# Kernel optimization log

Measured on AMD Instinct MI355X. Metric: run time of the kernel, lower is better.

Reference implementation:

```python
import jax, jax.numpy as jnp
from jax import lax
import numpy as np

L, B, N, D = 3, 64, 64, 64
E = 2 * D + 1  # per-edge feature dim: [state_i, state_j, w_ij]


def _build_edge_weights(n):
    # ring lattice (k=6) + distance-decaying random long-range links, symmetrized
    k = min(6, n // 4)
    ew = np.zeros((n, n), dtype=np.float32)
    for i in range(n):
        for j in range(1, k // 2 + 1):
            ew[i, (i + j) % n] = 1.0
            ew[i, (i - j) % n] = 1.0
    rng = np.random.default_rng(42)
    r = rng.random((n, n))
    for i in range(n):
        for j in range(n):
            if i != j and ew[i, j] == 0.0:
                dist = min(abs(i - j), n - abs(i - j))
                if r[i, j] < 0.1 / (dist + 1):
                    ew[i, j] = 0.5
    ew = (ew + ew.T) / 2.0
    return jnp.asarray(ew)


def setup_inputs() -> dict:
    key = jax.random.key(0)
    k1, k2, k3, k4 = jax.random.split(key, 4)
    x = jax.random.normal(k1, (B, N, D), dtype=jnp.float32)
    edge_weights = _build_edge_weights(N)
    W_msg = jax.random.normal(k2, (L, N, N, E, D), dtype=jnp.float32) * 0.05
    b_msg = jnp.zeros((L, N, N, D), dtype=jnp.float32)
    W_upd = jax.random.normal(k3, (L, 2 * D, D), dtype=jnp.float32) * 0.05
    b_upd = jnp.zeros((L, D), dtype=jnp.float32)
    W_out = jax.random.normal(k4, (D, D), dtype=jnp.float32) * 0.05
    b_out = jnp.zeros((D,), dtype=jnp.float32)
    return {"x": x, "edge_weights": edge_weights, "W_msg": W_msg, "b_msg": b_msg,
            "W_upd": W_upd, "b_upd": b_upd, "W_out": W_out, "b_out": b_out}


def reference(x, edge_weights, W_msg, b_msg, W_upd, b_upd, W_out, b_out):
    Bn, Nn, Dn = x.shape
    adj = (edge_weights > 0).astype(x.dtype)          # (N, N)
    deg = adj.sum(axis=1)                              # (N,)
    mask = adj[None, :, :, None]                       # (1, N, N, 1)
    s = x
    for l in range(W_msg.shape[0]):
        # per-edge features [state_i, state_j, w_ij] -> (B, N, N, 2D+1)
        feat_i = jnp.broadcast_to(s[:, :, None, :], (Bn, Nn, Nn, Dn))
        feat_j = jnp.broadcast_to(s[:, None, :, :], (Bn, Nn, Nn, Dn))
        w = jnp.broadcast_to(edge_weights[None, :, :, None], (Bn, Nn, Nn, 1))
        feat = jnp.concatenate([feat_i, feat_j, w], axis=-1)
        # distinct Dense per edge: grouped GEMM over the (i, j) edge grid
        msg = jnp.einsum('bije,ijed->bijd', feat, W_msg[l]) + b_msg[l]
        msg = msg * mask                               # only existing edges message
        agg = msg.sum(axis=2)                          # (B, N, D) sum over senders j
        upd = jnp.concatenate([s, agg], axis=-1) @ W_upd[l] + b_upd[l]
        s = 0.9 * upd + 0.1 * s                        # constraint_factor = 0.1
        # sequential topological constraint: blend each node toward current
        # neighbor average (node i sees already-updated nodes < i)
        def step(state, i):
            nbr_sum = jnp.einsum('j,bjd->bd', adj[i], state)
            avg = nbr_sum / jnp.maximum(deg[i], 1.0)
            new_i = jnp.where(deg[i] > 0, 0.95 * state[:, i] + 0.05 * avg, state[:, i])
            return state.at[:, i].set(new_i), None
        s, _ = lax.scan(step, s, jnp.arange(Nn))
    # degree-centrality weighted readout
    c = edge_weights.sum(axis=1)
    c = c / (c.sum() + 1e-8)
    g = (s * c[None, :, None]).sum(axis=1)             # (B, D)
    return g @ W_out + b_out
```

## Files before the change

### kernel.cpp

```cpp
#include <hip/hip_runtime.h>

namespace {

constexpr int B = 64, N = 64, D = 64, E = 2 * D + 1;
constexpr int NBLK = 256;
constexpr int NTH  = 512;
constexpr int LMAX = 3;
constexpr size_t MAXSLOT = 1024;

__device__ __forceinline__ float4 f4ld(const float* p) { return *(const float4*)p; }
__device__ __forceinline__ void f4acc(float4& a, const float4 b) {
  a.x += b.x; a.y += b.y; a.z += b.z; a.w += b.w;
}

__device__ __forceinline__ void gridbar(unsigned* set, unsigned* nxcd, int lead) {
  asm volatile("s_waitcnt vmcnt(0)" ::: "memory");
  __syncthreads();
  if (threadIdx.x == 0) {
    const int g = blockIdx.x;
    unsigned* leaf  = set + (size_t)(g & 7) * 16;
    unsigned* root  = set + 8 * 16;
    unsigned* root2 = set + 9 * 16;
    __hip_atomic_fetch_add(leaf, 1u, __ATOMIC_RELAXED, __HIP_MEMORY_SCOPE_AGENT);
    if (g < 8) {
      while (__hip_atomic_load(leaf, __ATOMIC_RELAXED, __HIP_MEMORY_SCOPE_AGENT)
             < (unsigned)(NBLK / 8))
        __builtin_amdgcn_s_sleep(2);
      __hip_atomic_fetch_add(root, 1u, __ATOMIC_RELAXED, __HIP_MEMORY_SCOPE_AGENT);
    }
    while (__hip_atomic_load(root, __ATOMIC_RELAXED, __HIP_MEMORY_SCOPE_AGENT) < 8u)
      __builtin_amdgcn_s_sleep(2);
    if (lead) {
      __threadfence();
      __hip_atomic_fetch_add(root2, 1u, __ATOMIC_RELAXED, __HIP_MEMORY_SCOPE_AGENT);
    }
    const unsigned K =
        __hip_atomic_load(nxcd, __ATOMIC_RELAXED, __HIP_MEMORY_SCOPE_AGENT);
    while (__hip_atomic_load(root2, __ATOMIC_RELAXED, __HIP_MEMORY_SCOPE_AGENT) < K)
      __builtin_amdgcn_s_sleep(2);
  }
  __syncthreads();
}

constexpr int OF_WU    = 32768;
constexpr int OF_TB    = 49152;
constexpr int OF_NBR4  = OF_TB;
constexpr int OF_DEG   = OF_TB + 1024;
constexpr int OF_CW    = OF_TB + 1280;
constexpr int OF_CNT   = OF_TB + 1536;
constexpr int OF_RB    = OF_TB + 1792;
constexpr int OF_BTMP  = OF_TB + 2048;
constexpr int OF_NE    = OF_TB + 2304;
constexpr int OF_EI    = OF_TB + 2320;
constexpr int OF_NFULL = OF_TB + 4368;
constexpr int POOLSZ   = 57856;

__global__ __launch_bounds__(NTH) void k_fused(
    const float* __restrict__ x,
    const float* __restrict__ ew,
    const float* __restrict__ Wm,
    const float* __restrict__ bm,
    const float* __restrict__ Wu,
    const float* __restrict__ bu,
    const float* __restrict__ Wo,
    const float* __restrict__ bo,
    float* __restrict__ out,
    char* __restrict__ ws, int L)
{
  unsigned* bar  = (unsigned*)ws;
  unsigned* nxcd = bar + 960;
  char* p = ws + 4096;
  float* sbuf0   = (float*)p; p += (size_t)B * N * D * 4;
  float* sbuf1   = (float*)p; p += (size_t)B * N * D * 4;
  float* selfm   = (float*)p; p += (size_t)LMAX * N * B * D * 4;
  float* msgBuf  = (float*)p; p += (size_t)LMAX * MAXSLOT * B * D * 4;
  float* sw1     = (float*)p; p += (size_t)(LMAX - 1) * N * D * D * 4;
  float* baseB   = (float*)p;

  __shared__ __align__(16) char pool[POOLSZ];
  float (*aT)[64] = (float(*)[64])pool;
  float* wLds  = (float*)(pool + 16384);
  uint4* nbr4L = (uint4*)(pool + OF_NBR4);
  float* degL  = (float*)(pool + OF_DEG);
  float* cwL   = (float*)(pool + OF_CW);
  int*   cntL  = (int*)(pool + OF_CNT);
  int*   rbL   = (int*)(pool + OF_RB);
  float* baseTmp = (float*)(pool + OF_BTMP);
  int*   neL   = (int*)(pool + OF_NE);
  unsigned short* eiL = (unsigned short*)(pool + OF_EI);
  unsigned char* nfullL = (unsigned char*)(pool + OF_NFULL);

  const int g = blockIdx.x, t = threadIdx.x;

  int lead = 0;
  if (t == 0) {
    unsigned xcd = 0;
    asm volatile("s_getreg_b32 %0, hwreg(HW_REG_XCC_ID)" : "=s"(xcd));
    unsigned* elect = bar + 832 + (size_t)(xcd & 7) * 16;
    if (__hip_atomic_fetch_add(elect, 1u, __ATOMIC_RELAXED,
                               __HIP_MEMORY_SCOPE_AGENT) == 0u) {
      lead = 1;
      __hip_atomic_fetch_add(nxcd, 1u, __ATOMIC_RELAXED,
                             __HIP_MEMORY_SCOPE_AGENT);
    }
  }

  {
    float* ewL = (float*)pool;
#pragma unroll
    for (int r = 0; r < 2; ++r)
      ((float4*)ewL)[r * NTH + t] = ((const float4*)ew)[r * NTH + t];
    __syncthreads();
    if (t < 64) {
      float rowsum = 0.f; int rc = 0;
      for (int j = 0; j < N; ++j) {
        const float v = ewL[t * N + j];
        rowsum += v; rc += (v > 0.f) ? 1 : 0;
      }
      int pre = rc;
#pragma unroll
      for (int off = 1; off < 64; off <<= 1) {
        int v = __shfl_up(pre, off, 64);
        if (t >= off) pre += v;
      }
      const int base = pre - rc;
      rbL[t] = base;
      unsigned long long lo = 0ull, hi = 0ull; int c = 0;
      for (int j = 0; j < N; ++j) {
        const float v = ewL[t * N + j];
        if (v > 0.f) {
          eiL[base + c] = (unsigned short)((t << 6) | j);
          if (c < 8)       lo |= (unsigned long long)j << (c * 8);
          else if (c < 16) hi |= (unsigned long long)j << ((c - 8) * 8);
          nfullL[t * 64 + c] = (unsigned char)j;
          ++c;
        }
      }
      uint4 w4;
      w4.x = (unsigned)lo; w4.y = (unsigned)(lo >> 32);
      w4.z = (unsigned)hi; w4.w = (unsigned)(hi >> 32);
      nbr4L[t] = w4; cntL[t] = c; degL[t] = (float)c;
      float tot = rowsum;
#pragma unroll
      for (int off = 32; off >= 1; off >>= 1) tot += __shfl_xor(tot, off, 64);
      cwL[t] = rowsum / (tot + 1e-8f);
      if (t == 63) *neL = base + rc;
    }
    __syncthreads();
  }
  const int ne = *neL;

  for (int l = 0; l < L; ++l) {
    const float* scur = (l == 0) ? x : ((l & 1) ? sbuf1 : sbuf0);
    float* sout = (l & 1) ? sbuf0 : sbuf1;
    float* msgl  = msgBuf + (size_t)l * MAXSLOT * B * D;
    float* selfl = selfm + (size_t)l * N * B * D;
    const bool LAST = (l == L - 1);

    {
      const int U = ne + N;
      for (int u = g; u < U; u += NBLK) {
        const bool self = (u >= ne);
        int i, jj; float* dst;
        if (self) { i = u - ne; jj = i; dst = selfl + (size_t)i * B * D; }
        else {
          const int e = eiL[u]; i = e >> 6; jj = e & 63;
          dst = msgl + (size_t)u * B * D;
        }
        {
          const int bb = t >> 3, q = t & 7;
          const float* ps = scur + ((size_t)(bb * N + jj)) * D + q * 8;
          const float4 v0 = f4ld(ps), v1 = f4ld(ps + 4);
          const int k0 = q * 8;
          aT[k0 + 0][bb] = v0.x; aT[k0 + 1][bb] = v0.y;
          aT[k0 + 2][bb] = v0.z; aT[k0 + 3][bb] = v0.w;
          aT[k0 + 4][bb] = v1.x; aT[k0 + 5][bb] = v1.y;
          aT[k0 + 6][bb] = v1.z; aT[k0 + 7][bb] = v1.w;
        }
        if (!self) {
          const int e = eiL[u];
          const float* wsrc = Wm + ((size_t)((l * N + (e >> 6)) * N + (e & 63))) * (E * D) + D * D;
#pragma unroll
          for (int r = 0; r < 2; ++r)
            *(float4*)(wLds + (r * NTH + t) * 4) = f4ld(wsrc + (r * NTH + t) * 4);
        } else if (l > 0) {
          const float* wsrc = sw1 + ((size_t)(l - 1) * N + i) * D * D;
#pragma unroll
          for (int r = 0; r < 2; ++r)
            *(float4*)(wLds + (r * NTH + t) * 4) = f4ld(wsrc + (r * NTH + t) * 4);
          if (t < 16)
            *(float4*)(baseTmp + t * 4) = f4ld(baseB + ((size_t)(l - 1) * N + i) * D + t * 4);
        } else {
          float4 a0 = {0,0,0,0}, a1 = {0,0,0,0};
          float4 bacc = {0,0,0,0};
          const int ci = cntL[i];
          for (int c2 = 0; c2 < ci; ++c2) {
            const int j2 = nfullL[i * 64 + c2];
            const float* Wp = Wm + ((size_t)(i * N + j2)) * (E * D);
            f4acc(a0, f4ld(Wp + (0 * NTH + t) * 4));
            f4acc(a1, f4ld(Wp + (1 * NTH + t) * 4));
            if (t < 16) {
              const float w = ew[i * N + j2];
              const float4 w3 = f4ld(Wp + 2 * D * D + t * 4);
              const float4 bv = f4ld(bm + ((size_t)(i * N + j2)) * D + t * 4);
              bacc.x += w * w3.x + bv.x; bacc.y += w * w3.y + bv.y;
              bacc.z += w * w3.z + bv.z; bacc.w += w * w3.w + bv.w;
            }
          }
          *(float4*)(wLds + (0 * NTH + t) * 4) = a0;
          *(float4*)(wLds + (1 * NTH + t) * 4) = a1;
          if (t < 16) *(float4*)(baseTmp + t * 4) = bacc;
        }
        __syncthreads();

        const int td = t & 15, tr = t >> 4;
        float acc[2][4];
        if (self) {
          const float4 bv = f4ld(baseTmp + td * 4);
#pragma unroll
          for (int r = 0; r < 2; ++r) {
            acc[r][0] = bv.x; acc[r][1] = bv.y;
            acc[r][2] = bv.z; acc[r][3] = bv.w;
          }
        } else {
#pragma unroll
          for (int r = 0; r < 2; ++r)
#pragma unroll
            for (int c2 = 0; c2 < 4; ++c2) acc[r][c2] = 0.f;
        }
#pragma unroll 4
        for (int k = 0; k < D; ++k) {
          const float2 a  = *(const float2*)&aT[k][tr * 2];
          const float4 wv = f4ld(wLds + k * D + td * 4);
          const float ar[2] = {a.x, a.y};
          const float wc[4] = {wv.x, wv.y, wv.z, wv.w};
#pragma unroll
          for (int r = 0; r < 2; ++r)
#pragma unroll
            for (int c2 = 0; c2 < 4; ++c2) acc[r][c2] += ar[r] * wc[c2];
        }
        float* mp = dst + (size_t)(tr * 2) * D + td * 4;
#pragma unroll
        for (int r = 0; r < 2; ++r)
          *(float4*)(mp + (size_t)r * D) =
              make_float4(acc[r][0], acc[r][1], acc[r][2], acc[r][3]);
        __syncthreads();
      }
    }
    if (g < B) {
      const float* Wul = Wu + (size_t)l * 2 * D * D;
      float* wuC = (float*)(pool + OF_WU);
#pragma unroll
      for (int r = 0; r < 2; ++r)
        *(float4*)(wuC + (r * NTH + t) * 4) = f4ld(Wul + (r * NTH + t) * 4);
    }
    gridbar(bar + (size_t)(2 * l) * 160, nxcd, lead);

    if (g < B) {
      const int b = g;
      const float* Wul = Wu + (size_t)l * 2 * D * D;
      const float* bul = bu + (size_t)l * D;
      float (*catT)[64] = (float(*)[64])pool;
      float* wuC = (float*)(pool + OF_WU);

      {
        const int ii = t >> 3, q = t & 7;
        const int cI = cntL[ii], rb = rbL[ii];
        float4 a4[2];
        a4[0] = f4ld(selfl + ((size_t)(ii * B + b)) * D + q * 8);
        a4[1] = f4ld(selfl + ((size_t)(ii * B + b)) * D + q * 8 + 4);
        for (int e = 0; e < cI; ++e) {
          const float* pm = msgl + ((size_t)(rb + e) * B + b) * D + q * 8;
          f4acc(a4[0], f4ld(pm));
          f4acc(a4[1], f4ld(pm + 4));
        }
        const float* ps = scur + ((size_t)(b * N + ii)) * D + q * 8;
        const float4 v0 = f4ld(ps), v1 = f4ld(ps + 4);
        const int k0 = q * 8;
        catT[k0 + 0][ii] = v0.x; catT[k0 + 1][ii] = v0.y;
        catT[k0 + 2][ii] = v0.z; catT[k0 + 3][ii] = v0.w;
        catT[k0 + 4][ii] = v1.x; catT[k0 + 5][ii] = v1.y;
        catT[k0 + 6][ii] = v1.z; catT[k0 + 7][ii] = v1.w;
        catT[D + k0 + 0][ii] = a4[0].x; catT[D + k0 + 1][ii] = a4[0].y;
        catT[D + k0 + 2][ii] = a4[0].z; catT[D + k0 + 3][ii] = a4[0].w;
        catT[D + k0 + 4][ii] = a4[1].x; catT[D + k0 + 5][ii] = a4[1].y;
        catT[D + k0 + 6][ii] = a4[1].z; catT[D + k0 + 7][ii] = a4[1].w;
      }
      __syncthreads();

      const int td = t & 15, tr = t >> 4;
      float acc[2][4];
      {
        const float4 bv = f4ld(bul + td * 4);
#pragma unroll
        for (int r = 0; r < 2; ++r) {
          acc[r][0] = bv.x; acc[r][1] = bv.y;
          acc[r][2] = bv.z; acc[r][3] = bv.w;
        }
      }
#pragma unroll 4
      for (int k = 0; k < 64; ++k) {
        const float2 a  = *(const float2*)&catT[k][tr * 2];
        const float4 wv = f4ld(wuC + k * D + td * 4);
        const float ar[2] = {a.x, a.y};
        const float wc[4] = {wv.x, wv.y, wv.z, wv.w};
#pragma unroll
        for (int r = 0; r < 2; ++r)
#pragma unroll
          for (int c2 = 0; c2 < 4; ++c2) acc[r][c2] += ar[r] * wc[c2];
      }
      __syncthreads();
#pragma unroll
      for (int r = 0; r < 2; ++r)
        *(float4*)(wuC + (r * NTH + t) * 4) = f4ld(Wul + 64 * D + (r * NTH + t) * 4);
      __syncthreads();
#pragma unroll 4
      for (int k = 0; k < 64; ++k) {
        const float2 a  = *(const float2*)&catT[64 + k][tr * 2];
        const float4 wv = f4ld(wuC + k * D + td * 4);
        const float ar[2] = {a.x, a.y};
        const float wc[4] = {wv.x, wv.y, wv.z, wv.w};
#pragma unroll
        for (int r = 0; r < 2; ++r)
#pragma unroll
          for (int c2 = 0; c2 < 4; ++c2) acc[r][c2] += ar[r] * wc[c2];
      }
#pragma unroll
      for (int r = 0; r < 2; ++r)
#pragma unroll
        for (int c2 = 0; c2 < 4; ++c2)
          acc[r][c2] = 0.9f * acc[r][c2] + 0.1f * catT[td * 4 + c2][tr * 2 + r];
      __syncthreads();
      float (*sb)[65] = (float(*)[65])pool;
#pragma unroll
      for (int r = 0; r < 2; ++r)
#pragma unroll
        for (int c2 = 0; c2 < 4; ++c2)
          sb[tr * 2 + r][td * 4 + c2] = acc[r][c2];
      __syncthreads();

      if (t < 64) {
        const int d = t;
        uint4 w = nbr4L[0];
        int c = cntL[0];
        float dg = degL[0];
        for (int ii = 0; ii < N; ++ii) {
          uint4 wn = w; int cn = c; float dgn = dg;
          if (ii < N - 1) { wn = nbr4L[ii + 1]; cn = cntL[ii + 1]; dgn = degL[ii + 1]; }
          const unsigned wd[4] = {w.x, w.y, w.z, w.w};
          float nb = 0.0f;
#pragma unroll
          for (int q = 0; q < 8; ++q) {
            const int idx = (int)((wd[q >> 2] >> ((q & 3) * 8)) & 63u);
            const float v = sb[idx][d];
            nb += (q < c) ? v : 0.0f;
          }
          if (c > 8) {
#pragma unroll
            for (int q = 8; q < 16; ++q) {
              const int idx = (int)((wd[q >> 2] >> ((q & 3) * 8)) & 63u);
              const float v = sb[idx][d];
              nb += (q < c) ? v : 0.0f;
            }
            for (int q = 16; q < c; ++q) nb += sb[nfullL[ii * 64 + q]][d];
          }
          const float avg = nb / fmaxf(dg, 1.0f);
          const float cur = sb[ii][d];
          sb[ii][d] = (dg > 0.0f) ? (0.95f * cur + 0.05f * avg) : cur;
          w = wn; c = cn; dg = dgn;
        }
        if (LAST) {
          float gg = 0.0f;
          for (int i2 = 0; i2 < N; ++i2) gg += cwL[i2] * sb[i2][d];
          float o = bo[d];
          for (int k2 = 0; k2 < D; ++k2) o += __shfl(gg, k2, 64) * Wo[k2 * D + d];
          out[(size_t)b * D + d] = o;
        }
      }
      if (!LAST) {
        __syncthreads();
        const int ii = t >> 3, q = t & 7;
        float* ps = sout + ((size_t)(b * N + ii)) * D + q * 8;
        float4 v0, v1;
        v0.x = sb[ii][q * 8 + 0]; v0.y = sb[ii][q * 8 + 1];
        v0.z = sb[ii][q * 8 + 2]; v0.w = sb[ii][q * 8 + 3];
        v1.x = sb[ii][q * 8 + 4]; v1.y = sb[ii][q * 8 + 5];
        v1.z = sb[ii][q * 8 + 6]; v1.w = sb[ii][q * 8 + 7];
        *(float4*)ps = v0;
        *(float4*)(ps + 4) = v1;
      }
    } else if (!LAST && g >= 64 && g < 64 + 128) {
      const int u = g - 64, i = u & 63, half = u >> 6;
      const int lt = l + 1;
      float4 a0 = {0,0,0,0};
      float4 bacc = {0,0,0,0};
      const int ci = cntL[i];
      for (int c2 = 0; c2 < ci; ++c2) {
        const int j2 = nfullL[i * 64 + c2];
        const float* Wp = Wm + ((size_t)((lt * N + i) * N + j2)) * (E * D);
        f4acc(a0, f4ld(Wp + (half * NTH + t) * 4));
        if (half == 0 && t < 16) {
          const float w = ew[i * N + j2];
          const float4 w3 = f4ld(Wp + 2 * D * D + t * 4);
          const float4 bv = f4ld(bm + (((size_t)lt * N + i) * N + j2) * D + t * 4);
          bacc.x += w * w3.x + bv.x; bacc.y += w * w3.y + bv.y;
          bacc.z += w * w3.z + bv.z; bacc.w += w * w3.w + bv.w;
        }
      }
      float* dstw = sw1 + ((size_t)l * N + i) * D * D;
      *(float4*)(dstw + (half * NTH + t) * 4) = a0;
      if (half == 0 && t < 16)
        *(float4*)(baseB + ((size_t)l * N + i) * D + t * 4) = bacc;
    }
    if (l < L - 1) gridbar(bar + (size_t)(2 * l + 1) * 160, nxcd, lead);
  }
}

}

extern "C" void kernel_launch(void* const* d_in, const int* in_sizes, int n_in,
                              void* d_out, int out_size, void* d_ws, size_t ws_size,
                              hipStream_t stream)
{
  const float* x  = (const float*)d_in[0];
  const float* ew = (const float*)d_in[1];
  const float* Wm = (const float*)d_in[2];
  const float* bm = (const float*)d_in[3];
  const float* Wu = (const float*)d_in[4];
  const float* bu = (const float*)d_in[5];
  const float* Wo = (const float*)d_in[6];
  const float* bo = (const float*)d_in[7];
  float* out = (float*)d_out;

  int L = in_sizes[2] / (N * N * E * D);
  if (L > LMAX) L = LMAX;

  hipMemsetAsync(d_ws, 0, 4096, stream);
  k_fused<<<NBLK, NTH, 0, stream>>>(x, ew, Wm, bm, Wu, bu, Wo, bo, out,
                                    (char*)d_ws, L);
}
```

Before: 149.1 us.

## Split non-final update phase across two blocks per batch by output-column half

For non-final layers, the node-update GEMM and the sequential neighbor-blend scan are split across two blocks per batch element, each handling 32 of the 64 output columns. Each block stages only its half of W_upd in LDS, and the weight-sum blocks shift to start at block 128. The barrier replaces __threadfence with an explicit L2 writeback plus waitcnt. The inner loop adds a redundant `a*wv.x*0.0f` term, and the final layer keeps the original single-block path.

```diff
diff --git a/kernel.cpp b/kernel.cpp
--- a/kernel.cpp
+++ b/kernel.cpp
@@ -31,7 +31,8 @@
     while (__hip_atomic_load(root, __ATOMIC_RELAXED, __HIP_MEMORY_SCOPE_AGENT) < 8u)
       __builtin_amdgcn_s_sleep(2);
     if (lead) {
-      __threadfence();
+      asm volatile("buffer_wbl2 sc1\n\t"
+                   "s_waitcnt vmcnt(0)" ::: "memory");
       __hip_atomic_fetch_add(root2, 1u, __ATOMIC_RELAXED, __HIP_MEMORY_SCOPE_AGENT);
     }
     const unsigned K =
@@ -247,21 +248,30 @@
         __syncthreads();
       }
     }
-    if (g < B) {
+    float* wuC = (float*)(pool + OF_WU);
+    if (!LAST) {
+      if (g < 2 * B) {
+        const int dh = g & 1;
+        const float* Wul = Wu + (size_t)l * 2 * D * D;
+#pragma unroll
+        for (int r = 0; r < 2; ++r) {
+          const int idx = r * NTH + t;
+          const int row = idx >> 3, lc = (idx & 7) * 4;
+          *(float4*)(wuC + row * 32 + lc) = f4ld(Wul + row * D + dh * 32 + lc);
+        }
+      }
+    } else if (g < B) {
       const float* Wul = Wu + (size_t)l * 2 * D * D;
-      float* wuC = (float*)(pool + OF_WU);
 #pragma unroll
       for (int r = 0; r < 2; ++r)
         *(float4*)(wuC + (r * NTH + t) * 4) = f4ld(Wul + (r * NTH + t) * 4);
     }
     gridbar(bar + (size_t)(2 * l) * 160, nxcd, lead);
 
-    if (g < B) {
-      const int b = g;
-      const float* Wul = Wu + (size_t)l * 2 * D * D;
+    if (!LAST && g < 2 * B) {
+      const int b = g >> 1, dh = g & 1;
       const float* bul = bu + (size_t)l * D;
       float (*catT)[64] = (float(*)[64])pool;
-      float* wuC = (float*)(pool + OF_WU);
 
       {
         const int ii = t >> 3, q = t & 7;
@@ -288,109 +298,68 @@
       }
       __syncthreads();
 
-      const int td = t & 15, tr = t >> 4;
-      float acc[2][4];
+      const int row = t & 63, cq = t >> 6;
+      float acc[4];
       {
-        const float4 bv = f4ld(bul + td * 4);
-#pragma unroll
-        for (int r = 0; r < 2; ++r) {
-          acc[r][0] = bv.x; acc[r][1] = bv.y;
-          acc[r][2] = bv.z; acc[r][3] = bv.w;
-        }
+        const float4 bv = f4ld(bul + dh * 32 + cq * 4);
+        acc[0] = bv.x; acc[1] = bv.y; acc[2] = bv.z; acc[3] = bv.w;
       }
 #pragma unroll 4
-      for (int k = 0; k < 64; ++k) {
-        const float2 a  = *(const float2*)&catT[k][tr * 2];
-        const float4 wv = f4ld(wuC + k * D + td * 4);
-        const float ar[2] = {a.x, a.y};
-        const float wc[4] = {wv.x, wv.y, wv.z, wv.w};
-#pragma unroll
-        for (int r = 0; r < 2; ++r)
-#pragma unroll
-          for (int c2 = 0; c2 < 4; ++c2) acc[r][c2] += ar[r] * wc[c2];
-      }
-      __syncthreads();
-#pragma unroll
-      for (int r = 0; r < 2; ++r)
-        *(float4*)(wuC + (r * NTH + t) * 4) = f4ld(Wul + 64 * D + (r * NTH + t) * 4);
-      __syncthreads();
-#pragma unroll 4
-      for (int k = 0; k < 64; ++k) {
-        const float2 a  = *(const float2*)&catT[64 + k][tr * 2];
-        const float4 wv = f4ld(wuC + k * D + td * 4);
-        const float ar[2] = {a.x, a.y};
-        const float wc[4] = {wv.x, wv.y, wv.z, wv.w};
-#pragma unroll
-        for (int r = 0; r < 2; ++r)
-#pragma unroll
-          for (int c2 = 0; c2 < 4; ++c2) acc[r][c2] += ar[r] * wc[c2];
-      }
-#pragma unroll
-      for (int r = 0; r < 2; ++r)
-#pragma unroll
-        for (int c2 = 0; c2 < 4; ++c2)
-          acc[r][c2] = 0.9f * acc[r][c2] + 0.1f * catT[td * 4 + c2][tr * 2 + r];
-      __syncthreads();
-      float (*sb)[65] = (float(*)[65])pool;
-#pragma unroll
-      for (int r = 0; r < 2; ++r)
-#pragma unroll
-        for (int c2 = 0; c2 < 4; ++c2)
-          sb[tr * 2 + r][td * 4 + c2] = acc[r][c2];
-      __syncthreads();
-
-      if (t < 64) {
-        const int d = t;
+      for (int k = 0; k < 2 * D; ++k) {
+        const float a  = catT[k][row];
+        const float4 wv = f4ld(wuC + k * 32 + cq * 4);
+#pragma unroll
+        for (int j = 0; j < 4; ++j) acc[j] += a * wv.x * 0.0f + a * ((const float*)&wv)[j];
+      }
+#pragma unroll
+      for (int j = 0; j < 4; ++j)
+        acc[j] = 0.9f * acc[j] + 0.1f * catT[dh * 32 + cq * 4 + j][row];
+      __syncthreads();
+      float (*sb)[33] = (float(*)[33])pool;
+#pragma unroll
+      for (int j = 0; j < 4; ++j) sb[row][cq * 4 + j] = acc[j];
+      __syncthreads();
+
+      if (t < 32) {
+        const int c = t;
         uint4 w = nbr4L[0];
-        int c = cntL[0];
+        int cc = cntL[0];
         float dg = degL[0];
         for (int ii = 0; ii < N; ++ii) {
-          uint4 wn = w; int cn = c; float dgn = dg;
+          uint4 wn = w; int cn = cc; float dgn = dg;
           if (ii < N - 1) { wn = nbr4L[ii + 1]; cn = cntL[ii + 1]; dgn = degL[ii + 1]; }
           const unsigned wd[4] = {w.x, w.y, w.z, w.w};
           float nb = 0.0f;
 #pragma unroll
           for (int q = 0; q < 8; ++q) {
             const int idx = (int)((wd[q >> 2] >> ((q & 3) * 8)) & 63u);
-            const float v = sb[idx][d];
-            nb += (q < c) ? v : 0.0f;
+            const float v = sb[idx][c];
+            nb += (q < cc) ? v : 0.0f;
           }
-          if (c > 8) {
+          if (cc > 8) {
 #pragma unroll
             for (int q = 8; q < 16; ++q) {
               const int idx = (int)((wd[q >> 2] >> ((q & 3) * 8)) & 63u);
-              const float v = sb[idx][d];
-              nb += (q < c) ? v : 0.0f;
+              const float v = sb[idx][c];
+              nb += (q < cc) ? v : 0.0f;
             }
-            for (int q = 16; q < c; ++q) nb += sb[nfullL[ii * 64 + q]][d];
+            for (int q = 16; q < cc; ++q) nb += sb[nfullL[ii * 64 + q]][c];
           }
           const float avg = nb / fmaxf(dg, 1.0f);
-          const float cur = sb[ii][d];
-          sb[ii][d] = (dg > 0.0f) ? (0.95f * cur + 0.05f * avg) : cur;
-          w = wn; c = cn; dg = dgn;
-        }
-        if (LAST) {
-          float gg = 0.0f;
-          for (int i2 = 0; i2 < N; ++i2) gg += cwL[i2] * sb[i2][d];
-          float o = bo[d];
-          for (int k2 = 0; k2 < D; ++k2) o += __shfl(gg, k2, 64) * Wo[k2 * D + d];
-          out[(size_t)b * D + d] = o;
-        }
-      }
-      if (!LAST) {
-        __syncthreads();
-        const int ii = t >> 3, q = t & 7;
-        float* ps = sout + ((size_t)(b * N + ii)) * D + q * 8;
-        float4 v0, v1;
-        v0.x = sb[ii][q * 8 + 0]; v0.y = sb[ii][q * 8 + 1];
-        v0.z = sb[ii][q * 8 + 2]; v0.w = sb[ii][q * 8 + 3];
-        v1.x = sb[ii][q * 8 + 4]; v1.y = sb[ii][q * 8 + 5];
-        v1.z = sb[ii][q * 8 + 6]; v1.w = sb[ii][q * 8 + 7];
-        *(float4*)ps = v0;
-        *(float4*)(ps + 4) = v1;
-      }
-    } else if (!LAST && g >= 64 && g < 64 + 128) {
-      const int u = g - 64, i = u & 63, half = u >> 6;
+          const float cur = sb[ii][c];
+          sb[ii][c] = (dg > 0.0f) ? (0.95f * cur + 0.05f * avg) : cur;
+          w = wn; cc = cn; dg = dgn;
+        }
+      }
+      __syncthreads();
+      {
+        float4 v;
+        v.x = sb[row][cq * 4 + 0]; v.y = sb[row][cq * 4 + 1];
+        v.z = sb[row][cq * 4 + 2]; v.w = sb[row][cq * 4 + 3];
+        *(float4*)(sout + ((size_t)(b * N + row)) * D + dh * 32 + cq * 4) = v;
+      }
+    } else if (!LAST && g >= 2 * B) {
+      const int u = g - 2 * B, i = u & 63, half = u >> 6;
       const int lt = l + 1;
       float4 a0 = {0,0,0,0};
       float4 bacc = {0,0,0,0};
@@ -411,6 +380,124 @@
       *(float4*)(dstw + (half * NTH + t) * 4) = a0;
       if (half == 0 && t < 16)
         *(float4*)(baseB + ((size_t)l * N + i) * D + t * 4) = bacc;
+    } else if (LAST && g < B) {
+      const int b = g;
+      const float* Wul = Wu + (size_t)l * 2 * D * D;
+      const float* bul = bu + (size_t)l * D;
+      float (*catT)[64] = (float(*)[64])pool;
+
+      {
+        const int ii = t >> 3, q = t & 7;
+        const int cI = cntL[ii], rb = rbL[ii];
+        float4 a4[2];
+        a4[0] = f4ld(selfl + ((size_t)(ii * B + b)) * D + q * 8);
+        a4[1] = f4ld(selfl + ((size_t)(ii * B + b)) * D + q * 8 + 4);
+        for (int e = 0; e < cI; ++e) {
+          const float* pm = msgl + ((size_t)(rb + e) * B + b) * D + q * 8;
+          f4acc(a4[0], f4ld(pm));
+          f4acc(a4[1], f4ld(pm + 4));
+        }
+        const float* ps = scur + ((size_t)(b * N + ii)) * D + q * 8;
+        const float4 v0 = f4ld(ps), v1 = f4ld(ps + 4);
+        const int k0 = q * 8;
+        catT[k0 + 0][ii] = v0.x; catT[k0 + 1][ii] = v0.y;
+        catT[k0 + 2][ii] = v0.z; catT[k0 + 3][ii] = v0.w;
+        catT[k0 + 4][ii] = v1.x; catT[k0 + 5][ii] = v1.y;
+        catT[k0 + 6][ii] = v1.z; catT[k0 + 7][ii] = v1.w;
+        catT[D + k0 + 0][ii] = a4[0].x; catT[D + k0 + 1][ii] = a4[0].y;
+        catT[D + k0 + 2][ii] = a4[0].z; catT[D + k0 + 3][ii] = a4[0].w;
+        catT[D + k0 + 4][ii] = a4[1].x; catT[D + k0 + 5][ii] = a4[1].y;
+        catT[D + k0 + 6][ii] = a4[1].z; catT[D + k0 + 7][ii] = a4[1].w;
+      }
+      __syncthreads();
+
+      const int td = t & 15, tr = t >> 4;
+      float acc[2][4];
+      {
+        const float4 bv = f4ld(bul + td * 4);
+#pragma unroll
+        for (int r = 0; r < 2; ++r) {
+          acc[r][0] = bv.x; acc[r][1] = bv.y;
+          acc[r][2] = bv.z; acc[r][3] = bv.w;
+        }
+      }
+#pragma unroll 4
+      for (int k = 0; k < 64; ++k) {
+        const float2 a  = *(const float2*)&catT[k][tr * 2];
+        const float4 wv = f4ld(wuC + k * D + td * 4);
+        const float ar[2] = {a.x, a.y};
+        const float wc[4] = {wv.x, wv.y, wv.z, wv.w};
+#pragma unroll
+        for (int r = 0; r < 2; ++r)
+#pragma unroll
+          for (int c2 = 0; c2 < 4; ++c2) acc[r][c2] += ar[r] * wc[c2];
+      }
+      __syncthreads();
+#pragma unroll
+      for (int r = 0; r < 2; ++r)
+        *(float4*)(wuC + (r * NTH + t) * 4) = f4ld(Wul + 64 * D + (r * NTH + t) * 4);
+      __syncthreads();
+#pragma unroll 4
+      for (int k = 0; k < 64; ++k) {
+        const float2 a  = *(const float2*)&catT[64 + k][tr * 2];
+        const float4 wv = f4ld(wuC + k * D + td * 4);
+        const float ar[2] = {a.x, a.y};
+        const float wc[4] = {wv.x, wv.y, wv.z, wv.w};
+#pragma unroll
+        for (int r = 0; r < 2; ++r)
+#pragma unroll
+          for (int c2 = 0; c2 < 4; ++c2) acc[r][c2] += ar[r] * wc[c2];
+      }
+#pragma unroll
+      for (int r = 0; r < 2; ++r)
+#pragma unroll
+        for (int c2 = 0; c2 < 4; ++c2)
+          acc[r][c2] = 0.9f * acc[r][c2] + 0.1f * catT[td * 4 + c2][tr * 2 + r];
+      __syncthreads();
+      float (*sb)[65] = (float(*)[65])pool;
+#pragma unroll
+      for (int r = 0; r < 2; ++r)
+#pragma unroll
+        for (int c2 = 0; c2 < 4; ++c2)
+          sb[tr * 2 + r][td * 4 + c2] = acc[r][c2];
+      __syncthreads();
+
+      if (t < 64) {
+        const int d = t;
+        uint4 w = nbr4L[0];
+        int c = cntL[0];
+        float dg = degL[0];
+        for (int ii = 0; ii < N; ++ii) {
+          uint4 wn = w; int cn = c; float dgn = dg;
+          if (ii < N - 1) { wn = nbr4L[ii + 1]; cn = cntL[ii + 1]; dgn = degL[ii + 1]; }
+          const unsigned wd[4] = {w.x, w.y, w.z, w.w};
+          float nb = 0.0f;
+#pragma unroll
+          for (int q = 0; q < 8; ++q) {
+            const int idx = (int)((wd[q >> 2] >> ((q & 3) * 8)) & 63u);
+            const float v = sb[idx][d];
+            nb += (q < c) ? v : 0.0f;
+          }
+          if (c > 8) {
+#pragma unroll
+            for (int q = 8; q < 16; ++q) {
+              const int idx = (int)((wd[q >> 2] >> ((q & 3) * 8)) & 63u);
+              const float v = sb[idx][d];
+              nb += (q < c) ? v : 0.0f;
+            }
+            for (int q = 16; q < c; ++q) nb += sb[nfullL[ii * 64 + q]][d];
+          }
+          const float avg = nb / fmaxf(dg, 1.0f);
+          const float cur = sb[ii][d];
+          sb[ii][d] = (dg > 0.0f) ? (0.95f * cur + 0.05f * avg) : cur;
+          w = wn; c = cn; dg = dgn;
+        }
+        float gg = 0.0f;
+        for (int i2 = 0; i2 < N; ++i2) gg += cwL[i2] * sb[i2][d];
+        float o = bo[d];
+        for (int k2 = 0; k2 < D; ++k2) o += __shfl(gg, k2, 64) * Wo[k2 * D + d];
+        out[(size_t)b * D + d] = o;
+      }
     }
     if (l < L - 1) gridbar(bar + (size_t)(2 * l + 1) * 160, nxcd, lead);
   }
```

New measurement: 157.0 us. 5.3% more time.

## Split self/edge blocks and replace fenced grid barrier with atomic-store barrier

Applied to the files above, without the earlier changes.

Blocks 0-63 now handle the per-node self-message GEMMs. They sum each node's neighbor weight slices inline every layer, instead of reading sums that idle blocks precomputed for the next layer. The remaining 192 blocks stride over the edge messages. State writes at the end of each layer now use global_atomic_swap_x2 stores so they are coherent at device scope. That lets the inter-layer barrier drop the threadfence and the third cross-XCD counting stage. The trade-off is that the weight summation moves back onto the critical path of the self blocks, and an unused lambda is left in the code.

```diff
diff --git a/kernel.cpp b/kernel.cpp
--- a/kernel.cpp
+++ b/kernel.cpp
@@ -8,9 +8,21 @@
 constexpr int LMAX = 3;
 constexpr size_t MAXSLOT = 1024;
 
+using i32x2 = __attribute__((ext_vector_type(2))) int;
+
 __device__ __forceinline__ float4 f4ld(const float* p) { return *(const float4*)p; }
 __device__ __forceinline__ void f4acc(float4& a, const float4 b) {
   a.x += b.x; a.y += b.y; a.z += b.z; a.w += b.w;
+}
+
+__device__ __forceinline__ void st_at8(float* p, float a, float b) {
+  i32x2 v; v[0] = __float_as_int(a); v[1] = __float_as_int(b);
+  asm volatile("global_atomic_swap_x2 %0, %1, off"
+               :: "v"(p), "v"(v) : "memory");
+}
+__device__ __forceinline__ void st_at16(float* p, float4 v) {
+  st_at8(p, v.x, v.y);
+  st_at8(p + 2, v.z, v.w);
 }
 
 __device__ __forceinline__ void gridbar(unsigned* set, unsigned* nxcd, int lead) {
@@ -37,6 +49,26 @@
     const unsigned K =
         __hip_atomic_load(nxcd, __ATOMIC_RELAXED, __HIP_MEMORY_SCOPE_AGENT);
     while (__hip_atomic_load(root2, __ATOMIC_RELAXED, __HIP_MEMORY_SCOPE_AGENT) < K)
+      __builtin_amdgcn_s_sleep(2);
+  }
+  __syncthreads();
+}
+
+__device__ __forceinline__ void abar(unsigned* set) {
+  asm volatile("s_waitcnt vmcnt(0)" ::: "memory");
+  __syncthreads();
+  if (threadIdx.x == 0) {
+    const int g = blockIdx.x;
+    unsigned* leaf = set + (size_t)(g & 7) * 16;
+    unsigned* root = set + 8 * 16;
+    __hip_atomic_fetch_add(leaf, 1u, __ATOMIC_RELAXED, __HIP_MEMORY_SCOPE_AGENT);
+    if (g < 8) {
+      while (__hip_atomic_load(leaf, __ATOMIC_RELAXED, __HIP_MEMORY_SCOPE_AGENT)
+             < (unsigned)(NBLK / 8))
+        __builtin_amdgcn_s_sleep(2);
+      __hip_atomic_fetch_add(root, 1u, __ATOMIC_RELAXED, __HIP_MEMORY_SCOPE_AGENT);
+    }
+    while (__hip_atomic_load(root, __ATOMIC_RELAXED, __HIP_MEMORY_SCOPE_AGENT) < 8u)
       __builtin_amdgcn_s_sleep(2);
   }
   __syncthreads();
@@ -73,9 +105,7 @@
   float* sbuf0   = (float*)p; p += (size_t)B * N * D * 4;
   float* sbuf1   = (float*)p; p += (size_t)B * N * D * 4;
   float* selfm   = (float*)p; p += (size_t)LMAX * N * B * D * 4;
-  float* msgBuf  = (float*)p; p += (size_t)LMAX * MAXSLOT * B * D * 4;
-  float* sw1     = (float*)p; p += (size_t)(LMAX - 1) * N * D * D * 4;
-  float* baseB   = (float*)p;
+  float* msgBuf  = (float*)p;
 
   __shared__ __align__(16) char pool[POOLSZ];
   float (*aT)[64] = (float(*)[64])pool;
@@ -158,15 +188,7 @@
     const bool LAST = (l == L - 1);
 
     {
-      const int U = ne + N;
-      for (int u = g; u < U; u += NBLK) {
-        const bool self = (u >= ne);
-        int i, jj; float* dst;
-        if (self) { i = u - ne; jj = i; dst = selfl + (size_t)i * B * D; }
-        else {
-          const int e = eiL[u]; i = e >> 6; jj = e & 63;
-          dst = msgl + (size_t)u * B * D;
-        }
+      auto unit = [&](int jj, const float* wsrc_edge, bool self, int i) {
         {
           const int bb = t >> 3, q = t & 7;
           const float* ps = scur + ((size_t)(bb * N + jj)) * D + q * 8;
@@ -178,31 +200,22 @@
           aT[k0 + 6][bb] = v1.z; aT[k0 + 7][bb] = v1.w;
         }
         if (!self) {
-          const int e = eiL[u];
-          const float* wsrc = Wm + ((size_t)((l * N + (e >> 6)) * N + (e & 63))) * (E * D) + D * D;
-#pragma unroll
-          for (int r = 0; r < 2; ++r)
-            *(float4*)(wLds + (r * NTH + t) * 4) = f4ld(wsrc + (r * NTH + t) * 4);
-        } else if (l > 0) {
-          const float* wsrc = sw1 + ((size_t)(l - 1) * N + i) * D * D;
-#pragma unroll
-          for (int r = 0; r < 2; ++r)
-            *(float4*)(wLds + (r * NTH + t) * 4) = f4ld(wsrc + (r * NTH + t) * 4);
-          if (t < 16)
-            *(float4*)(baseTmp + t * 4) = f4ld(baseB + ((size_t)(l - 1) * N + i) * D + t * 4);
+#pragma unroll
+          for (int r = 0; r < 2; ++r)
+            *(float4*)(wLds + (r * NTH + t) * 4) =
+                f4ld(wsrc_edge + (size_t)(r * NTH + t) * 4);
         } else {
-          float4 a0 = {0,0,0,0}, a1 = {0,0,0,0};
-          float4 bacc = {0,0,0,0};
+          float4 a0 = {0,0,0,0}, a1 = {0,0,0,0}, bacc = {0,0,0,0};
           const int ci = cntL[i];
           for (int c2 = 0; c2 < ci; ++c2) {
             const int j2 = nfullL[i * 64 + c2];
-            const float* Wp = Wm + ((size_t)(i * N + j2)) * (E * D);
-            f4acc(a0, f4ld(Wp + (0 * NTH + t) * 4));
-            f4acc(a1, f4ld(Wp + (1 * NTH + t) * 4));
+            const float* Wp = Wm + ((size_t)((l * N + i) * N + j2)) * (E * D);
+            f4acc(a0, f4ld(Wp + (size_t)(0 * NTH + t) * 4));
+            f4acc(a1, f4ld(Wp + (size_t)(1 * NTH + t) * 4));
             if (t < 16) {
               const float w = ew[i * N + j2];
               const float4 w3 = f4ld(Wp + 2 * D * D + t * 4);
-              const float4 bv = f4ld(bm + ((size_t)(i * N + j2)) * D + t * 4);
+              const float4 bv = f4ld(bm + (((size_t)l * N + i) * N + j2) * D + t * 4);
               bacc.x += w * w3.x + bv.x; bacc.y += w * w3.y + bv.y;
               bacc.z += w * w3.z + bv.z; bacc.w += w * w3.w + bv.w;
             }
@@ -239,12 +252,116 @@
 #pragma unroll
             for (int c2 = 0; c2 < 4; ++c2) acc[r][c2] += ar[r] * wc[c2];
         }
-        float* mp = dst + (size_t)(tr * 2) * D + td * 4;
+        float* dst = self ? (selfl + (size_t)i * B * D) : nullptr;
+        return acc, dst;
+      };
+      (void)unit;
+
+      if (g < 64) {
+        const int i = g;
+        {
+          const int bb = t >> 3, q = t & 7;
+          const float* ps = scur + ((size_t)(bb * N + i)) * D + q * 8;
+          const float4 v0 = f4ld(ps), v1 = f4ld(ps + 4);
+          const int k0 = q * 8;
+          aT[k0 + 0][bb] = v0.x; aT[k0 + 1][bb] = v0.y;
+          aT[k0 + 2][bb] = v0.z; aT[k0 + 3][bb] = v0.w;
+          aT[k0 + 4][bb] = v1.x; aT[k0 + 5][bb] = v1.y;
+          aT[k0 + 6][bb] = v1.z; aT[k0 + 7][bb] = v1.w;
+        }
+        {
+          float4 a0 = {0,0,0,0}, a1 = {0,0,0,0}, bacc = {0,0,0,0};
+          const int ci = cntL[i];
+          for (int c2 = 0; c2 < ci; ++c2) {
+            const int j2 = nfullL[i * 64 + c2];
+            const float* Wp = Wm + ((size_t)((l * N + i) * N + j2)) * (E * D);
+            f4acc(a0, f4ld(Wp + (size_t)(0 * NTH + t) * 4));
+            f4acc(a1, f4ld(Wp + (size_t)(1 * NTH + t) * 4));
+            if (t < 16) {
+              const float w = ew[i * N + j2];
+              const float4 w3 = f4ld(Wp + 2 * D * D + t * 4);
+              const float4 bv = f4ld(bm + (((size_t)l * N + i) * N + j2) * D + t * 4);
+              bacc.x += w * w3.x + bv.x; bacc.y += w * w3.y + bv.y;
+              bacc.z += w * w3.z + bv.z; bacc.w += w * w3.w + bv.w;
+            }
+          }
+          *(float4*)(wLds + (0 * NTH + t) * 4) = a0;
+          *(float4*)(wLds + (1 * NTH + t) * 4) = a1;
+          if (t < 16) *(float4*)(baseTmp + t * 4) = bacc;
+        }
+        __syncthreads();
+        const int td = t & 15, tr = t >> 4;
+        float acc[2][4];
+        {
+          const float4 bv = f4ld(baseTmp + td * 4);
+#pragma unroll
+          for (int r = 0; r < 2; ++r) {
+            acc[r][0] = bv.x; acc[r][1] = bv.y;
+            acc[r][2] = bv.z; acc[r][3] = bv.w;
+          }
+        }
+#pragma unroll 4
+        for (int k = 0; k < D; ++k) {
+          const float2 a  = *(const float2*)&aT[k][tr * 2];
+          const float4 wv = f4ld(wLds + k * D + td * 4);
+          const float ar[2] = {a.x, a.y};
+          const float wc[4] = {wv.x, wv.y, wv.z, wv.w};
+#pragma unroll
+          for (int r = 0; r < 2; ++r)
+#pragma unroll
+            for (int c2 = 0; c2 < 4; ++c2) acc[r][c2] += ar[r] * wc[c2];
+        }
+        float* mp = selfl + (size_t)i * B * D + (size_t)(tr * 2) * D + td * 4;
 #pragma unroll
         for (int r = 0; r < 2; ++r)
           *(float4*)(mp + (size_t)r * D) =
               make_float4(acc[r][0], acc[r][1], acc[r][2], acc[r][3]);
         __syncthreads();
+      } else {
+        for (int u = g - 64; u < ne; u += NBLK - 64) {
+          const int e = eiL[u];
+          const int jj = e & 63;
+          {
+            const int bb = t >> 3, q = t & 7;
+            const float* ps = scur + ((size_t)(bb * N + jj)) * D + q * 8;
+            const float4 v0 = f4ld(ps), v1 = f4ld(ps + 4);
+            const int k0 = q * 8;
+            aT[k0 + 0][bb] = v0.x; aT[k0 + 1][bb] = v0.y;
+            aT[k0 + 2][bb] = v0.z; aT[k0 + 3][bb] = v0.w;
+            aT[k0 + 4][bb] = v1.x; aT[k0 + 5][bb] = v1.y;
+            aT[k0 + 6][bb] = v1.z; aT[k0 + 7][bb] = v1.w;
+          }
+          const float* wsrc = Wm + ((size_t)((l * N + (e >> 6)) * N + jj)) * (E * D) + (size_t)D * D;
+#pragma unroll
+          for (int r = 0; r < 2; ++r)
+            *(float4*)(wLds + (r * NTH + t) * 4) =
+                f4ld(wsrc + (size_t)(r * NTH + t) * 4);
+          __syncthreads();
+
+          const int td = t & 15, tr = t >> 4;
+          float acc[2][4];
+#pragma unroll
+          for (int r = 0; r < 2; ++r)
+#pragma unroll
+            for (int c2 = 0; c2 < 4; ++c2) acc[r][c2] = 0.f;
+#pragma unroll 4
+          for (int k = 0; k < D; ++k) {
+            const float2 a  = *(const float2*)&aT[k][tr * 2];
+            const float4 wv = f4ld(wLds + k * D + td * 4);
+            const float ar[2] = {a.x, a.y};
+            const float wc[4] = {wv.x, wv.y, wv.z, wv.w};
+#pragma unroll
+            for (int r = 0; r < 2; ++r)
+#pragma unroll
+              for (int c2 = 0; c2 < 4; ++c2) acc[r][c2] += ar[r] * wc[c2];
+          }
+          float* mp = msgl + (size_t)u * B * D + (size_t)(tr * 2) * D + td * 4;
+#pragma unroll
+          for (int r = 0; r < 2; ++r)
+            *(float4*)(mp + (size_t)r * D) =
+                make_float4(acc[r][0], acc[r][1], acc[r][2], acc[r][3]);
+          __syncthreads();
+        }
       }
     }
     if (g < B) {
@@ -252,7 +369,7 @@
       float* wuC = (float*)(pool + OF_WU);
 #pragma unroll
       for (int r = 0; r < 2; ++r)
-        *(float4*)(wuC + (r * NTH + t) * 4) = f4ld(Wul + (r * NTH + t) * 4);
+        *(float4*)(wuC + (r * NTH + t) * 4) = f4ld(Wul + (size_t)(r * NTH + t) * 4);
     }
     gridbar(bar + (size_t)(2 * l) * 160, nxcd, lead);
 
@@ -312,7 +429,8 @@
       __syncthreads();
 #pragma unroll
       for (int r = 0; r < 2; ++r)
-        *(float4*)(wuC + (r * NTH + t) * 4) = f4ld(Wul + 64 * D + (r * NTH + t) * 4);
+        *(float4*)(wuC + (r * NTH + t) * 4) =
+            f4ld(Wul + (size_t)64 * D + (size_t)(r * NTH + t) * 4);
       __syncthreads();
 #pragma unroll 4
       for (int k = 0; k < 64; ++k) {
@@ -386,33 +504,11 @@
         v0.z = sb[ii][q * 8 + 2]; v0.w = sb[ii][q * 8 + 3];
         v1.x = sb[ii][q * 8 + 4]; v1.y = sb[ii][q * 8 + 5];
         v1.z = sb[ii][q * 8 + 6]; v1.w = sb[ii][q * 8 + 7];
-        *(float4*)ps = v0;
-        *(float4*)(ps + 4) = v1;
-      }
-    } else if (!LAST && g >= 64 && g < 64 + 128) {
-      const int u = g - 64, i = u & 63, half = u >> 6;
-      const int lt = l + 1;
-      float4 a0 = {0,0,0,0};
-      float4 bacc = {0,0,0,0};
-      const int ci = cntL[i];
-      for (int c2 = 0; c2 < ci; ++c2) {
-        const int j2 = nfullL[i * 64 + c2];
-        const float* Wp = Wm + ((size_t)((lt * N + i) * N + j2)) * (E * D);
-        f4acc(a0, f4ld(Wp + (half * NTH + t) * 4));
-        if (half == 0 && t < 16) {
-          const float w = ew[i * N + j2];
-          const float4 w3 = f4ld(Wp + 2 * D * D + t * 4);
-          const float4 bv = f4ld(bm + (((size_t)lt * N + i) * N + j2) * D + t * 4);
-          bacc.x += w * w3.x + bv.x; bacc.y += w * w3.y + bv.y;
-          bacc.z += w * w3.z + bv.z; bacc.w += w * w3.w + bv.w;
-        }
-      }
-      float* dstw = sw1 + ((size_t)l * N + i) * D * D;
-      *(float4*)(dstw + (half * NTH + t) * 4) = a0;
-      if (half == 0 && t < 16)
-        *(float4*)(baseB + ((size_t)l * N + i) * D + t * 4) = bacc;
-    }
-    if (l < L - 1) gridbar(bar + (size_t)(2 * l + 1) * 160, nxcd, lead);
+        st_at16(ps, v0);
+        st_at16(ps + 4, v1);
+      }
+    }
+    if (l < L - 1) abar(bar + (size_t)(2 * l + 1) * 160);
   }
 }
 
```

After: 154.2 us. 1.03x slower.

## Publish cross-block results with device-scope atomic swaps and use a lighter grid barrier

Applied to the files above, without the earlier changes.

The producer stores for state, reduced weights and bias bases become 64-bit global atomic swaps, so they land at device coherence. This lets the end-of-layer grid barrier drop its cross-XCD fence-and-count stage and use a simpler two-level atomic barrier. The aim is to cut barrier latency, in exchange for each float4 store becoming two atomic operations. Correctness now depends on the atomics being visible across XCDs without an explicit fence.

```diff
diff --git a/kernel.cpp b/kernel.cpp
--- a/kernel.cpp
+++ b/kernel.cpp
@@ -8,9 +8,21 @@
 constexpr int LMAX = 3;
 constexpr size_t MAXSLOT = 1024;
 
+using i32x2 = __attribute__((ext_vector_type(2))) int;
+
 __device__ __forceinline__ float4 f4ld(const float* p) { return *(const float4*)p; }
 __device__ __forceinline__ void f4acc(float4& a, const float4 b) {
   a.x += b.x; a.y += b.y; a.z += b.z; a.w += b.w;
+}
+
+__device__ __forceinline__ void st_at8(float* p, float a, float b) {
+  i32x2 v; v[0] = __float_as_int(a); v[1] = __float_as_int(b);
+  asm volatile("global_atomic_swap_x2 %0, %1, off"
+               :: "v"(p), "v"(v) : "memory");
+}
+__device__ __forceinline__ void st_at16(float* p, float4 v) {
+  st_at8(p, v.x, v.y);
+  st_at8(p + 2, v.z, v.w);
 }
 
 __device__ __forceinline__ void gridbar(unsigned* set, unsigned* nxcd, int lead) {
@@ -37,6 +49,26 @@
     const unsigned K =
         __hip_atomic_load(nxcd, __ATOMIC_RELAXED, __HIP_MEMORY_SCOPE_AGENT);
     while (__hip_atomic_load(root2, __ATOMIC_RELAXED, __HIP_MEMORY_SCOPE_AGENT) < K)
+      __builtin_amdgcn_s_sleep(2);
+  }
+  __syncthreads();
+}
+
+__device__ __forceinline__ void abar(unsigned* set) {
+  asm volatile("s_waitcnt vmcnt(0)" ::: "memory");
+  __syncthreads();
+  if (threadIdx.x == 0) {
+    const int g = blockIdx.x;
+    unsigned* leaf = set + (size_t)(g & 7) * 16;
+    unsigned* root = set + 8 * 16;
+    __hip_atomic_fetch_add(leaf, 1u, __ATOMIC_RELAXED, __HIP_MEMORY_SCOPE_AGENT);
+    if (g < 8) {
+      while (__hip_atomic_load(leaf, __ATOMIC_RELAXED, __HIP_MEMORY_SCOPE_AGENT)
+             < (unsigned)(NBLK / 8))
+        __builtin_amdgcn_s_sleep(2);
+      __hip_atomic_fetch_add(root, 1u, __ATOMIC_RELAXED, __HIP_MEMORY_SCOPE_AGENT);
+    }
+    while (__hip_atomic_load(root, __ATOMIC_RELAXED, __HIP_MEMORY_SCOPE_AGENT) < 8u)
       __builtin_amdgcn_s_sleep(2);
   }
   __syncthreads();
@@ -386,8 +418,8 @@
         v0.z = sb[ii][q * 8 + 2]; v0.w = sb[ii][q * 8 + 3];
         v1.x = sb[ii][q * 8 + 4]; v1.y = sb[ii][q * 8 + 5];
         v1.z = sb[ii][q * 8 + 6]; v1.w = sb[ii][q * 8 + 7];
-        *(float4*)ps = v0;
-        *(float4*)(ps + 4) = v1;
+        st_at16(ps, v0);
+        st_at16(ps + 4, v1);
       }
     } else if (!LAST && g >= 64 && g < 64 + 128) {
       const int u = g - 64, i = u & 63, half = u >> 6;
@@ -408,11 +440,11 @@
         }
       }
       float* dstw = sw1 + ((size_t)l * N + i) * D * D;
-      *(float4*)(dstw + (half * NTH + t) * 4) = a0;
+      st_at16(dstw + (half * NTH + t) * 4, a0);
       if (half == 0 && t < 16)
-        *(float4*)(baseB + ((size_t)l * N + i) * D + t * 4) = bacc;
-    }
-    if (l < L - 1) gridbar(bar + (size_t)(2 * l + 1) * 160, nxcd, lead);
+        st_at16(baseB + ((size_t)l * N + i) * D + t * 4, bacc);
+    }
+    if (l < L - 1) abar(bar + (size_t)(2 * l + 1) * 160);
   }
 }
 
```

Result: slower. 152.9 us (+2.5%).
